# Kernel tuning notes

Measured on AMD Instinct MI355X. Metric: run time of the kernel, lower is better.

## Reference

```python
import jax, jax.numpy as jnp
import numpy as np

B, T, OBS, H, A, S = 4096, 64, 64, 64, 8, 201


def setup_inputs() -> dict:
    key = jax.random.key(0)
    ks = jax.random.split(key, 13)
    n = lambda k, shp, s=1.0: jax.random.normal(k, shp, dtype=jnp.float32) * s
    return {
        "x": n(ks[0], (B, T, OBS)),
        "stack": jnp.zeros((B, S, H), jnp.float32),
        "stack_ptrs": jax.random.randint(ks[1], (B, 1), 0, 100, dtype=jnp.int32),
        # core_network: init.normal_(std=1.0) per source
        "W1": n(ks[2], (H, OBS + H)), "b1": n(ks[3], (H,)),
        "W2": n(ks[4], (H, H)), "b2": n(ks[5], (H,)),
        # stack_head: default torch Linear init ~ U(-1/sqrt(H), 1/sqrt(H))
        "Ws": (jax.random.uniform(ks[6], (3, H), dtype=jnp.float32) * 2 - 1) / np.sqrt(H),
        "bs": (jax.random.uniform(ks[7], (3,), dtype=jnp.float32) * 2 - 1) / np.sqrt(H),
        # policy/value heads: init.normal_(std=0.01)
        "Wp": n(ks[8], (A, H), 0.01), "bp": n(ks[9], (A,), 0.01),
        "Wv": n(ks[10], (1, H), 0.01), "bv": n(ks[11], (1,), 0.01),
    }


def reference(x, stack, stack_ptrs, W1, b1, W2, b2, Ws, bs, Wp, bp, Wv, bv):
    # x: [B,T,OBS]  stack: [B,S,H]  stack_ptrs: [B,1] int
    batch = x.shape[0]
    bidx = jnp.arange(batch)
    ptrs0 = stack_ptrs.astype(jnp.int32)[:, 0]  # [B]

    def step(carry, x_t):
        stk, ptrs = carry
        top = stk[bidx, ptrs]                                   # [B,H] gather at ptr
        h = jnp.tanh(jnp.concatenate([x_t, top], axis=1) @ W1.T + b1)
        p = jnp.tanh(h @ W2.T + b2)                             # [B,H]
        probs = jax.nn.softmax(p @ Ws.T + bs, axis=1)           # [B,3]
        ops = jnp.argmax(probs, axis=1).astype(jnp.int32)       # 0=pop,1=noop,2=push
        push = (ops == 2)[:, None]
        # conditional scatter: write p at row ptr only where op==2
        stk = stk.at[bidx, ptrs].set(jnp.where(push, p, top))
        ptrs = jnp.maximum(ptrs + ops - 1, 0)
        logits = p @ Wp.T + bp                                  # [B,A]
        value = (p @ Wv.T + bv)[:, 0]                           # [B]
        return (stk, ptrs), (logits, value)

    (stack_out, ptrs_out), (logits_t, values_t) = jax.lax.scan(
        step, (stack, ptrs0), jnp.swapaxes(x, 0, 1))
    logitss = jnp.swapaxes(logits_t, 0, 1)      # [B,T,A]
    values = values_t.reshape(-1)               # time-major [T*B], matching torch layout
    return logitss, values, stack_out, ptrs_out[:, None]
```

## Files before the change

### kernel.cpp

```cpp
#include <hip/hip_runtime.h>
#include <cstddef>

#define NB 4096
#define NT 64
#define NOBS 64
#define NH 64
#define NA 8
#define NS 201


__global__ void copy_stack_kernel(const float4* __restrict__ src,
                                  float4* __restrict__ dst, int n4) {
    int i = blockIdx.x * blockDim.x + threadIdx.x;
    int stride = gridDim.x * blockDim.x;
    for (; i < n4; i += stride) dst[i] = src[i];
}

__launch_bounds__(256, 2)
__global__ void stacknet_kernel(const float* __restrict__ x,
                                const int* __restrict__ ptrs_in,
                                const float* __restrict__ W1,
                                const float* __restrict__ b1,
                                const float* __restrict__ W2,
                                const float* __restrict__ b2,
                                const float* __restrict__ Ws,
                                const float* __restrict__ bs,
                                const float* __restrict__ Wp,
                                const float* __restrict__ bp,
                                const float* __restrict__ Wv,
                                const float* __restrict__ bv,
                                float* __restrict__ logits_out,
                                float* __restrict__ values_out,
                                float* __restrict__ stack,
                                float* __restrict__ ptrs_out) {
    const int lane = threadIdx.x & 63;
    const int wv = threadIdx.x >> 6;
    const int b = (blockIdx.x << 2) + wv;
    const int aa = lane & 15;

    __shared__ float shwT[64 * 16];
    __shared__ float shb[16];
    __shared__ float vbuf[4][192];
    __shared__ float pbuf[4][64];

    for (int i = threadIdx.x; i < 64 * 16; i += 256) {
        int k = i >> 4, a = i & 15;
        float w = 0.0f;
        if (a < 3)       w = Ws[a * 64 + k];
        else if (a < 11) w = Wp[(a - 3) * 64 + k];
        else if (a == 11) w = Wv[k];
        shwT[i] = w;
    }
    if (threadIdx.x < 16) {
        int a = threadIdx.x;
        float bb = 0.0f;
        if (a < 3) bb = bs[a];
        else if (a < 11) bb = bp[a - 3];
        else if (a == 11) bb = bv[0];
        shb[a] = bb;
    }
    __syncthreads();

    float w1r[128];
#pragma unroll
    for (int j = 0; j < 32; ++j) {
        float4 tW = ((const float4*)W1)[lane * 32 + j];
        w1r[4*j] = tW.x; w1r[4*j+1] = tW.y; w1r[4*j+2] = tW.z; w1r[4*j+3] = tW.w;
    }
    float w2r[64];
#pragma unroll
    for (int j = 0; j < 16; ++j) {
        float4 tW = ((const float4*)W2)[lane * 16 + j];
        w2r[4*j] = tW.x; w2r[4*j+1] = tW.y; w2r[4*j+2] = tW.z; w2r[4*j+3] = tW.w;
    }
    float b1r = b1[lane];
    float b2r = b2[lane];

    int ptr = ptrs_in[b];
    const float* xb  = x + (size_t)b * NT * NOBS;
    float* stk       = stack + (size_t)b * NS * NH;
    float* lgb       = logits_out + (size_t)b * NT * NA;

    for (int t = 0; t < NT; ++t) {
        float xv = xb[t * 64 + lane];
        float tv = stk[ptr * 64 + lane];
        vbuf[wv][lane]      = xv;
        vbuf[wv][64 + lane] = tv;

        float acc = 0.0f;
        const float4* vb4 = (const float4*)(&vbuf[wv][0]);
#pragma unroll
        for (int j = 0; j < 32; ++j) {
            float4 v = vb4[j];
            acc = fmaf(w1r[4*j],   v.x, acc);
            acc = fmaf(w1r[4*j+1], v.y, acc);
            acc = fmaf(w1r[4*j+2], v.z, acc);
            acc = fmaf(w1r[4*j+3], v.w, acc);
        }
        float h = tanhf(acc + b1r);
        vbuf[wv][128 + lane] = h;

        float acc2 = 0.0f;
        const float4* hb4 = (const float4*)(&vbuf[wv][128]);
#pragma unroll
        for (int j = 0; j < 16; ++j) {
            float4 v = hb4[j];
            acc2 = fmaf(w2r[4*j],   v.x, acc2);
            acc2 = fmaf(w2r[4*j+1], v.y, acc2);
            acc2 = fmaf(w2r[4*j+2], v.z, acc2);
            acc2 = fmaf(w2r[4*j+3], v.w, acc2);
        }
        float p = tanhf(acc2 + b2r);
        pbuf[wv][lane] = p;

        float hacc = 0.0f;
#pragma unroll
        for (int k = 0; k < 64; ++k) {
            hacc = fmaf(pbuf[wv][k], shwT[k * 16 + aa], hacc);
        }
        float sv = hacc + shb[aa];

        float s0 = __shfl(sv, 0, 64);
        float s1 = __shfl(sv, 1, 64);
        float s2 = __shfl(sv, 2, 64);

        float m = fmaxf(fmaxf(s0, s1), s2);
        float e0 = expf(s0 - m);
        float e1 = expf(s1 - m);
        float e2 = expf(s2 - m);
        float S = (e0 + e1) + e2;
        float p0 = e0 / S, p1 = e1 / S, p2 = e2 / S;
        int op = 0;
        float pm = p0;
        if (p1 > pm) { pm = p1; op = 1; }
        if (p2 > pm) { op = 2; }

        if (op == 2) stk[ptr * 64 + lane] = p;
        ptr = ptr + op - 1;
        if (ptr < 0) ptr = 0;

        if (lane >= 3 && lane <= 10) {
            lgb[t * NA + (lane - 3)] = sv;
        }
        if (lane == 11) {
            values_out[(size_t)t * NB + b] = sv;
        }
    }
    if (lane == 0) ptrs_out[b] = (float)ptr;
}

extern "C" void kernel_launch(void* const* d_in, const int* in_sizes, int n_in,
                              void* d_out, int out_size, void* d_ws, size_t ws_size,
                              hipStream_t stream) {
    const float* x        = (const float*)d_in[0];
    const float* stack_in = (const float*)d_in[1];
    const int*   ptrs_in  = (const int*)d_in[2];
    const float* W1 = (const float*)d_in[3];
    const float* b1 = (const float*)d_in[4];
    const float* W2 = (const float*)d_in[5];
    const float* b2 = (const float*)d_in[6];
    const float* Ws = (const float*)d_in[7];
    const float* bs = (const float*)d_in[8];
    const float* Wp = (const float*)d_in[9];
    const float* bp = (const float*)d_in[10];
    const float* Wv = (const float*)d_in[11];
    const float* bv = (const float*)d_in[12];

    float* out      = (float*)d_out;
    float* logits   = out;
    float* values   = out + 2097152;
    float* stack    = out + 2359296;
    float* ptrs_out = out + 55050240;

    int n4 = 52690944 / 4;
    copy_stack_kernel<<<4096, 256, 0, stream>>>((const float4*)stack_in,
                                                (float4*)stack, n4);
    stacknet_kernel<<<1024, 256, 0, stream>>>(x, ptrs_in, W1, b1, W2, b2,
                                              Ws, bs, Wp, bp, Wv, bv,
                                              logits, values, stack, ptrs_out);
}
```

Before: 774.1 us.

## Interleave two batch rows per wave and speculatively prefetch stack rows

Each wavefront now processes two independent batch elements in lockstep, reusing the register-resident W1/W2 weights for both and halving the grid. The next timestep's x and the three candidate stack rows (ptr-1, ptr, ptr+1) are loaded before the op decision, with a forwarded push value for pop-after-push. This takes the dependent global load off the serial critical path. Head weights are stored row-major with padding for float4 LDS reads. The trade-off is fewer resident waves, extra speculative loads, and more live registers.

```diff
diff --git a/kernel.cpp b/kernel.cpp
--- a/kernel.cpp
+++ b/kernel.cpp
@@ -35,21 +35,21 @@
                                 float* __restrict__ ptrs_out) {
     const int lane = threadIdx.x & 63;
     const int wv = threadIdx.x >> 6;
-    const int b = (blockIdx.x << 2) + wv;
+    const int bA = (blockIdx.x << 2) + wv;
+    const int bB = bA + 2048;
     const int aa = lane & 15;
 
-    __shared__ float shwT[64 * 16];
+    __shared__ __align__(16) float shw[16 * 68];
     __shared__ float shb[16];
-    __shared__ float vbuf[4][192];
-    __shared__ float pbuf[4][64];
-
-    for (int i = threadIdx.x; i < 64 * 16; i += 256) {
-        int k = i >> 4, a = i & 15;
+    __shared__ __align__(16) float vbuf[4][2][256];
+
+    for (int i = threadIdx.x; i < 16 * 64; i += 256) {
+        int a = i >> 6, k = i & 63;
         float w = 0.0f;
-        if (a < 3)       w = Ws[a * 64 + k];
-        else if (a < 11) w = Wp[(a - 3) * 64 + k];
+        if (a < 3)        w = Ws[a * 64 + k];
+        else if (a < 11)  w = Wp[(a - 3) * 64 + k];
         else if (a == 11) w = Wv[k];
-        shwT[i] = w;
+        shw[a * 68 + k] = w;
     }
     if (threadIdx.x < 16) {
         int a = threadIdx.x;
@@ -76,77 +76,156 @@
     float b1r = b1[lane];
     float b2r = b2[lane];
 
-    int ptr = ptrs_in[b];
-    const float* xb  = x + (size_t)b * NT * NOBS;
-    float* stk       = stack + (size_t)b * NS * NH;
-    float* lgb       = logits_out + (size_t)b * NT * NA;
+    int ptrA = ptrs_in[bA];
+    int ptrB = ptrs_in[bB];
+    const float* xbA = x + (size_t)bA * NT * NOBS;
+    const float* xbB = x + (size_t)bB * NT * NOBS;
+    float* stkA = stack + (size_t)bA * NS * NH;
+    float* stkB = stack + (size_t)bB * NS * NH;
+    float* lgbA = logits_out + (size_t)bA * NT * NA;
+    float* lgbB = logits_out + (size_t)bB * NT * NA;
+
+    float* vA = &vbuf[wv][0][0];
+    float* vB = &vbuf[wv][1][0];
+    const float* shwa = &shw[aa * 68];
+    const float shba = shb[aa];
+
+    float topA = stkA[ptrA * 64 + lane];
+    float topB = stkB[ptrB * 64 + lane];
+    float xA = xbA[lane];
+    float xB = xbB[lane];
+
+    bool pushedA = false, pushedB = false;
+    float pushvalA = 0.0f, pushvalB = 0.0f;
 
     for (int t = 0; t < NT; ++t) {
-        float xv = xb[t * 64 + lane];
-        float tv = stk[ptr * 64 + lane];
-        vbuf[wv][lane]      = xv;
-        vbuf[wv][64 + lane] = tv;
-
-        float acc = 0.0f;
-        const float4* vb4 = (const float4*)(&vbuf[wv][0]);
+        int r0A = (ptrA > 0) ? (ptrA - 1) : 0;
+        int r0B = (ptrB > 0) ? (ptrB - 1) : 0;
+        float c0A = stkA[r0A * 64 + lane];
+        float c1A = stkA[ptrA * 64 + lane];
+        float c2A = stkA[(ptrA + 1) * 64 + lane];
+        float c0B = stkB[r0B * 64 + lane];
+        float c1B = stkB[ptrB * 64 + lane];
+        float c2B = stkB[(ptrB + 1) * 64 + lane];
+        int tn = (t + 1 < NT) ? (t + 1) : t;
+        float xnA = xbA[tn * 64 + lane];
+        float xnB = xbB[tn * 64 + lane];
+
+        vA[lane]      = xA;
+        vA[64 + lane] = topA;
+        vB[lane]      = xB;
+        vB[64 + lane] = topB;
+
+        float accA = 0.0f, accB = 0.0f;
+        const float4* vA4 = (const float4*)vA;
+        const float4* vB4 = (const float4*)vB;
 #pragma unroll
         for (int j = 0; j < 32; ++j) {
-            float4 v = vb4[j];
-            acc = fmaf(w1r[4*j],   v.x, acc);
-            acc = fmaf(w1r[4*j+1], v.y, acc);
-            acc = fmaf(w1r[4*j+2], v.z, acc);
-            acc = fmaf(w1r[4*j+3], v.w, acc);
-        }
-        float h = tanhf(acc + b1r);
-        vbuf[wv][128 + lane] = h;
-
-        float acc2 = 0.0f;
-        const float4* hb4 = (const float4*)(&vbuf[wv][128]);
+            float4 a4 = vA4[j];
+            float4 b4 = vB4[j];
+            accA = fmaf(w1r[4*j],   a4.x, accA);
+            accA = fmaf(w1r[4*j+1], a4.y, accA);
+            accA = fmaf(w1r[4*j+2], a4.z, accA);
+            accA = fmaf(w1r[4*j+3], a4.w, accA);
+            accB = fmaf(w1r[4*j],   b4.x, accB);
+            accB = fmaf(w1r[4*j+1], b4.y, accB);
+            accB = fmaf(w1r[4*j+2], b4.z, accB);
+            accB = fmaf(w1r[4*j+3], b4.w, accB);
+        }
+        float hA = tanhf(accA + b1r);
+        float hB = tanhf(accB + b1r);
+        vA[128 + lane] = hA;
+        vB[128 + lane] = hB;
+
+        float a2A = 0.0f, a2B = 0.0f;
+        const float4* hA4 = (const float4*)(vA + 128);
+        const float4* hB4 = (const float4*)(vB + 128);
 #pragma unroll
         for (int j = 0; j < 16; ++j) {
-            float4 v = hb4[j];
-            acc2 = fmaf(w2r[4*j],   v.x, acc2);
-            acc2 = fmaf(w2r[4*j+1], v.y, acc2);
-            acc2 = fmaf(w2r[4*j+2], v.z, acc2);
-            acc2 = fmaf(w2r[4*j+3], v.w, acc2);
-        }
-        float p = tanhf(acc2 + b2r);
-        pbuf[wv][lane] = p;
-
-        float hacc = 0.0f;
-#pragma unroll
-        for (int k = 0; k < 64; ++k) {
-            hacc = fmaf(pbuf[wv][k], shwT[k * 16 + aa], hacc);
-        }
-        float sv = hacc + shb[aa];
-
-        float s0 = __shfl(sv, 0, 64);
-        float s1 = __shfl(sv, 1, 64);
-        float s2 = __shfl(sv, 2, 64);
-
-        float m = fmaxf(fmaxf(s0, s1), s2);
-        float e0 = expf(s0 - m);
-        float e1 = expf(s1 - m);
-        float e2 = expf(s2 - m);
-        float S = (e0 + e1) + e2;
-        float p0 = e0 / S, p1 = e1 / S, p2 = e2 / S;
-        int op = 0;
-        float pm = p0;
-        if (p1 > pm) { pm = p1; op = 1; }
-        if (p2 > pm) { op = 2; }
-
-        if (op == 2) stk[ptr * 64 + lane] = p;
-        ptr = ptr + op - 1;
-        if (ptr < 0) ptr = 0;
+            float4 a4 = hA4[j];
+            float4 b4 = hB4[j];
+            a2A = fmaf(w2r[4*j],   a4.x, a2A);
+            a2A = fmaf(w2r[4*j+1], a4.y, a2A);
+            a2A = fmaf(w2r[4*j+2], a4.z, a2A);
+            a2A = fmaf(w2r[4*j+3], a4.w, a2A);
+            a2B = fmaf(w2r[4*j],   b4.x, a2B);
+            a2B = fmaf(w2r[4*j+1], b4.y, a2B);
+            a2B = fmaf(w2r[4*j+2], b4.z, a2B);
+            a2B = fmaf(w2r[4*j+3], b4.w, a2B);
+        }
+        float pA = tanhf(a2A + b2r);
+        float pB = tanhf(a2B + b2r);
+        vA[192 + lane] = pA;
+        vB[192 + lane] = pB;
+
+        float haccA = 0.0f, haccB = 0.0f;
+        const float4* pA4 = (const float4*)(vA + 192);
+        const float4* pB4 = (const float4*)(vB + 192);
+#pragma unroll
+        for (int j = 0; j < 16; ++j) {
+            float4 w4 = *(const float4*)(shwa + 4*j);
+            float4 a4 = pA4[j];
+            float4 b4 = pB4[j];
+            haccA = fmaf(a4.x, w4.x, haccA);
+            haccA = fmaf(a4.y, w4.y, haccA);
+            haccA = fmaf(a4.z, w4.z, haccA);
+            haccA = fmaf(a4.w, w4.w, haccA);
+            haccB = fmaf(b4.x, w4.x, haccB);
+            haccB = fmaf(b4.y, w4.y, haccB);
+            haccB = fmaf(b4.z, w4.z, haccB);
+            haccB = fmaf(b4.w, w4.w, haccB);
+        }
+        float svA = haccA + shba;
+        float svB = haccB + shba;
+
+        float s0A = __shfl(svA, 0, 64), s1A = __shfl(svA, 1, 64), s2A = __shfl(svA, 2, 64);
+        float s0B = __shfl(svB, 0, 64), s1B = __shfl(svB, 1, 64), s2B = __shfl(svB, 2, 64);
+
+        float mA = fmaxf(fmaxf(s0A, s1A), s2A);
+        float e0A = expf(s0A - mA), e1A = expf(s1A - mA), e2A = expf(s2A - mA);
+        float SA = (e0A + e1A) + e2A;
+        float p0A = e0A / SA, p1A = e1A / SA, p2A = e2A / SA;
+        int opA = 0; float pmA = p0A;
+        if (p1A > pmA) { pmA = p1A; opA = 1; }
+        if (p2A > pmA) { opA = 2; }
+
+        float mB = fmaxf(fmaxf(s0B, s1B), s2B);
+        float e0B = expf(s0B - mB), e1B = expf(s1B - mB), e2B = expf(s2B - mB);
+        float SB = (e0B + e1B) + e2B;
+        float p0B = e0B / SB, p1B = e1B / SB, p2B = e2B / SB;
+        int opB = 0; float pmB = p0B;
+        if (p1B > pmB) { pmB = p1B; opB = 1; }
+        if (p2B > pmB) { opB = 2; }
+
+        if (opA == 2) stkA[ptrA * 64 + lane] = pA;
+        if (opB == 2) stkB[ptrB * 64 + lane] = pB;
+
+        float selA = (opA == 0) ? c0A : ((opA == 1) ? c1A : c2A);
+        if (opA == 0 && pushedA) selA = pushvalA;
+        float selB = (opB == 0) ? c0B : ((opB == 1) ? c1B : c2B);
+        if (opB == 0 && pushedB) selB = pushvalB;
+
+        pushedA = (opA == 2); pushvalA = pA;
+        pushedB = (opB == 2); pushvalB = pB;
+
+        int nA = ptrA + opA - 1; ptrA = (nA < 0) ? 0 : nA;
+        int nB = ptrB + opB - 1; ptrB = (nB < 0) ? 0 : nB;
+        topA = selA; topB = selB;
+        xA = xnA; xB = xnB;
 
         if (lane >= 3 && lane <= 10) {
-            lgb[t * NA + (lane - 3)] = sv;
+            lgbA[t * NA + (lane - 3)] = svA;
+            lgbB[t * NA + (lane - 3)] = svB;
         }
         if (lane == 11) {
-            values_out[(size_t)t * NB + b] = sv;
-        }
-    }
-    if (lane == 0) ptrs_out[b] = (float)ptr;
+            values_out[(size_t)t * NB + bA] = svA;
+            values_out[(size_t)t * NB + bB] = svB;
+        }
+    }
+    if (lane == 0) {
+        ptrs_out[bA] = (float)ptrA;
+        ptrs_out[bB] = (float)ptrB;
+    }
 }
 
 extern "C" void kernel_launch(void* const* d_in, const int* in_sizes, int n_in,
@@ -175,7 +254,7 @@
     int n4 = 52690944 / 4;
     copy_stack_kernel<<<4096, 256, 0, stream>>>((const float4*)stack_in,
                                                 (float4*)stack, n4);
-    stacknet_kernel<<<1024, 256, 0, stream>>>(x, ptrs_in, W1, b1, W2, b2,
-                                              Ws, bs, Wp, bp, Wv, bv,
-                                              logits, values, stack, ptrs_out);
+    stacknet_kernel<<<512, 256, 0, stream>>>(x, ptrs_in, W1, b1, W2, b2,
+                                             Ws, bs, Wp, bp, Wv, bv,
+                                             logits, values, stack, ptrs_out);
 }
```

Result: slower. 1.826 ms (+135.9%).

## Prefetch candidate stack rows to take the dependent gather off the recurrence

Applied to the files above, without the earlier changes.

Each step now loads the stack rows at ptr-1 and ptr+1 ahead of time. After the argmax it picks the next top from registers (c0, the current top, c2, or the value just pushed) instead of doing a global load that depends on the updated pointer. This is meant to remove global-memory latency from the serial 64-step chain, at the cost of two extra loads per step. The head weights are also stored transposed with padding so the head dot product reads float4 from shared memory. The stack copy kernel now launches one thread per float4 instead of using a grid-stride loop.

```diff
diff --git a/kernel.cpp b/kernel.cpp
--- a/kernel.cpp
+++ b/kernel.cpp
@@ -12,8 +12,7 @@
 __global__ void copy_stack_kernel(const float4* __restrict__ src,
                                   float4* __restrict__ dst, int n4) {
     int i = blockIdx.x * blockDim.x + threadIdx.x;
-    int stride = gridDim.x * blockDim.x;
-    for (; i < n4; i += stride) dst[i] = src[i];
+    if (i < n4) dst[i] = src[i];
 }
 
 __launch_bounds__(256, 2)
@@ -38,18 +37,17 @@
     const int b = (blockIdx.x << 2) + wv;
     const int aa = lane & 15;
 
-    __shared__ float shwT[64 * 16];
+    __shared__ __align__(16) float shw[16 * 68];
     __shared__ float shb[16];
-    __shared__ float vbuf[4][192];
-    __shared__ float pbuf[4][64];
+    __shared__ __align__(16) float vbuf[4][256];
 
-    for (int i = threadIdx.x; i < 64 * 16; i += 256) {
-        int k = i >> 4, a = i & 15;
+    for (int i = threadIdx.x; i < 16 * 64; i += 256) {
+        int a = i >> 6, k = i & 63;
         float w = 0.0f;
-        if (a < 3)       w = Ws[a * 64 + k];
-        else if (a < 11) w = Wp[(a - 3) * 64 + k];
+        if (a < 3)        w = Ws[a * 64 + k];
+        else if (a < 11)  w = Wp[(a - 3) * 64 + k];
         else if (a == 11) w = Wv[k];
-        shwT[i] = w;
+        shw[a * 68 + k] = w;
     }
     if (threadIdx.x < 16) {
         int a = threadIdx.x;
@@ -81,63 +79,81 @@
     float* stk       = stack + (size_t)b * NS * NH;
     float* lgb       = logits_out + (size_t)b * NT * NA;
 
+    float* v = &vbuf[wv][0];
+    const float* shwa = &shw[aa * 68];
+    const float shba = shb[aa];
+
+    float top = stk[ptr * 64 + lane];
+    bool pushed = false;
+    float pushval = 0.0f;
+
     for (int t = 0; t < NT; ++t) {
+        int r0 = (ptr > 0) ? (ptr - 1) : 0;
+        float c0 = stk[r0 * 64 + lane];
+        float c2 = stk[(ptr + 1) * 64 + lane];
         float xv = xb[t * 64 + lane];
-        float tv = stk[ptr * 64 + lane];
-        vbuf[wv][lane]      = xv;
-        vbuf[wv][64 + lane] = tv;
+
+        v[lane]      = xv;
+        v[64 + lane] = top;
 
         float acc = 0.0f;
-        const float4* vb4 = (const float4*)(&vbuf[wv][0]);
+        const float4* v4 = (const float4*)v;
 #pragma unroll
         for (int j = 0; j < 32; ++j) {
-            float4 v = vb4[j];
-            acc = fmaf(w1r[4*j],   v.x, acc);
-            acc = fmaf(w1r[4*j+1], v.y, acc);
-            acc = fmaf(w1r[4*j+2], v.z, acc);
-            acc = fmaf(w1r[4*j+3], v.w, acc);
+            float4 a4 = v4[j];
+            acc = fmaf(w1r[4*j],   a4.x, acc);
+            acc = fmaf(w1r[4*j+1], a4.y, acc);
+            acc = fmaf(w1r[4*j+2], a4.z, acc);
+            acc = fmaf(w1r[4*j+3], a4.w, acc);
         }
         float h = tanhf(acc + b1r);
-        vbuf[wv][128 + lane] = h;
+        v[128 + lane] = h;
 
         float acc2 = 0.0f;
-        const float4* hb4 = (const float4*)(&vbuf[wv][128]);
+        const float4* h4 = (const float4*)(v + 128);
 #pragma unroll
         for (int j = 0; j < 16; ++j) {
-            float4 v = hb4[j];
-            acc2 = fmaf(w2r[4*j],   v.x, acc2);
-            acc2 = fmaf(w2r[4*j+1], v.y, acc2);
-            acc2 = fmaf(w2r[4*j+2], v.z, acc2);
-            acc2 = fmaf(w2r[4*j+3], v.w, acc2);
+            float4 a4 = h4[j];
+            acc2 = fmaf(w2r[4*j],   a4.x, acc2);
+            acc2 = fmaf(w2r[4*j+1], a4.y, acc2);
+            acc2 = fmaf(w2r[4*j+2], a4.z, acc2);
+            acc2 = fmaf(w2r[4*j+3], a4.w, acc2);
         }
         float p = tanhf(acc2 + b2r);
-        pbuf[wv][lane] = p;
+        v[192 + lane] = p;
 
         float hacc = 0.0f;
+        const float4* p4 = (const float4*)(v + 192);
 #pragma unroll
-        for (int k = 0; k < 64; ++k) {
-            hacc = fmaf(pbuf[wv][k], shwT[k * 16 + aa], hacc);
+        for (int j = 0; j < 16; ++j) {
+            float4 w4 = *(const float4*)(shwa + 4*j);
+            float4 a4 = p4[j];
+            hacc = fmaf(a4.x, w4.x, hacc);
+            hacc = fmaf(a4.y, w4.y, hacc);
+            hacc = fmaf(a4.z, w4.z, hacc);
+            hacc = fmaf(a4.w, w4.w, hacc);
         }
-        float sv = hacc + shb[aa];
+        float sv = hacc + shba;
 
-        float s0 = __shfl(sv, 0, 64);
-        float s1 = __shfl(sv, 1, 64);
-        float s2 = __shfl(sv, 2, 64);
-
+        float s0 = __shfl(sv, 0, 64), s1 = __shfl(sv, 1, 64), s2 = __shfl(sv, 2, 64);
         float m = fmaxf(fmaxf(s0, s1), s2);
-        float e0 = expf(s0 - m);
-        float e1 = expf(s1 - m);
-        float e2 = expf(s2 - m);
+        float e0 = expf(s0 - m), e1 = expf(s1 - m), e2 = expf(s2 - m);
         float S = (e0 + e1) + e2;
         float p0 = e0 / S, p1 = e1 / S, p2 = e2 / S;
-        int op = 0;
-        float pm = p0;
+        int op = 0; float pm = p0;
         if (p1 > pm) { pm = p1; op = 1; }
         if (p2 > pm) { op = 2; }
 
         if (op == 2) stk[ptr * 64 + lane] = p;
-        ptr = ptr + op - 1;
-        if (ptr < 0) ptr = 0;
+
+        float sel = (op == 0) ? (pushed ? pushval : c0)
+                              : ((op == 1) ? top : c2);
+        pushed = (op == 2);
+        pushval = p;
+
+        int np = ptr + op - 1;
+        ptr = (np < 0) ? 0 : np;
+        top = sel;
 
         if (lane >= 3 && lane <= 10) {
             lgb[t * NA + (lane - 3)] = sv;
@@ -173,8 +189,8 @@
     float* ptrs_out = out + 55050240;
 
     int n4 = 52690944 / 4;
-    copy_stack_kernel<<<4096, 256, 0, stream>>>((const float4*)stack_in,
-                                                (float4*)stack, n4);
+    copy_stack_kernel<<<51456, 256, 0, stream>>>((const float4*)stack_in,
+                                                 (float4*)stack, n4);
     stacknet_kernel<<<1024, 256, 0, stream>>>(x, ptrs_in, W1, b1, W2, b2,
                                               Ws, bs, Wp, bp, Wv, bv,
                                               logits, values, stack, ptrs_out);
```

After: 742.8 us. -4.0%, faster.
